# Performance work log

Hardware: AMD Instinct MI355X
Metric: run time of the kernel (lower is better)

Reference implementation:

```python
import jax, jax.numpy as jnp
import numpy as np

B, T, N, F_IN, F_OUT, H = 32, 32, 256, 32, 32, 256
NEG_SLOPE = 0.2  # GATConv default leaky-relu slope


def setup_inputs() -> dict:
    key = jax.random.key(0)
    ks = jax.random.split(key, 12)
    x = jax.random.normal(ks[0], (B, T, N, F_IN), dtype=jnp.float32)
    u = jax.random.uniform(ks[1], (B, T, N, N))
    w = jax.random.uniform(ks[2], (B, T, N, N))
    adj = jnp.where(u < 0.1, w, 0.0).astype(jnp.float32)
    # GAT params (heads=1, concat=False)
    W = jax.random.normal(ks[3], (F_IN, F_OUT), dtype=jnp.float32) / np.sqrt(F_IN)
    a_src = jax.random.normal(ks[4], (F_OUT,), dtype=jnp.float32) / np.sqrt(F_OUT)
    a_dst = jax.random.normal(ks[5], (F_OUT,), dtype=jnp.float32) / np.sqrt(F_OUT)
    gat_b = jnp.zeros((F_OUT,), dtype=jnp.float32)
    # LSTM params (PyTorch layout, gate order i,f,g,o)
    IN = N * F_OUT
    s = 1.0 / np.sqrt(H)
    W_ih = jax.random.uniform(ks[6], (4 * H, IN), minval=-s, maxval=s, dtype=jnp.float32)
    W_hh = jax.random.uniform(ks[7], (4 * H, H), minval=-s, maxval=s, dtype=jnp.float32)
    b_ih = jax.random.uniform(ks[8], (4 * H,), minval=-s, maxval=s, dtype=jnp.float32)
    b_hh = jax.random.uniform(ks[9], (4 * H,), minval=-s, maxval=s, dtype=jnp.float32)
    # output Linear
    Wo = jax.random.uniform(ks[10], (N, H), minval=-s, maxval=s, dtype=jnp.float32)
    bo = jax.random.uniform(ks[11], (N,), minval=-s, maxval=s, dtype=jnp.float32)
    return {"x": x, "adj": adj, "W": W, "a_src": a_src, "a_dst": a_dst,
            "gat_b": gat_b, "W_ih": W_ih, "W_hh": W_hh, "b_ih": b_ih,
            "b_hh": b_hh, "Wo": Wo, "bo": bo}


def _gat(x, adj, W, a_src, a_dst, gat_b):
    # batched over (B,T). h: [B,T,N,F_OUT]
    h = jnp.einsum('btnf,fo->btno', x, W)
    s_src = jnp.einsum('btno,o->btn', h, a_src)  # contribution of source node j
    s_dst = jnp.einsum('btno,o->btn', h, a_dst)  # contribution of target node i
    # e[i,j] = LeakyReLU(a_dst.h_i + a_src.h_j)
    e = jax.nn.leaky_relu(s_dst[..., :, None] + s_src[..., None, :], NEG_SLOPE)
    # edge (row=j -> col=i) exists iff adj[j,i] != 0; GATConv adds self-loops
    mask = (jnp.swapaxes(adj, -1, -2) != 0) | jnp.eye(N, dtype=bool)
    alpha = jax.nn.softmax(jnp.where(mask, e, -jnp.inf), axis=-1)  # softmax over sources j per target i
    return jnp.einsum('btij,btjo->btio', alpha, h) + gat_b


def _lstm_last(seq, W_ih, W_hh, b_ih, b_hh):
    # seq: [B,T,IN] -> last hidden state [B,H]
    def step(carry, x_t):
        h_prev, c_prev = carry
        gates = x_t @ W_ih.T + h_prev @ W_hh.T + (b_ih + b_hh)
        i, f, g, o = jnp.split(gates, 4, axis=-1)
        c = jax.nn.sigmoid(f) * c_prev + jax.nn.sigmoid(i) * jnp.tanh(g)
        h = jax.nn.sigmoid(o) * jnp.tanh(c)
        return (h, c), None
    init = (jnp.zeros((seq.shape[0], H), seq.dtype), jnp.zeros((seq.shape[0], H), seq.dtype))
    (h_last, _), _ = jax.lax.scan(step, init, jnp.swapaxes(seq, 0, 1))
    return h_last


def reference(x, adj, W, a_src, a_dst, gat_b, W_ih, W_hh, b_ih, b_hh, Wo, bo):
    gat_out = _gat(x, adj, W, a_src, a_dst, gat_b)            # [B,T,N,F_OUT]
    seq = gat_out.reshape(gat_out.shape[0], gat_out.shape[1], -1)  # [B,T,N*F_OUT]
    h_last = _lstm_last(seq, W_ih, W_hh, b_ih, b_hh)          # [B,H]
    return h_last @ Wo.T + bo                                  # [B,N]
```

## Files before the change

kernel.cpp:

```cpp
#include <hip/hip_runtime.h>
#include <cstdint>

constexpr int B_ = 32, T_ = 32, N_ = 256, FIN = 32, FOUT = 32, H_ = 256;
constexpr int IN_ = N_ * FOUT;
constexpr int G4  = 4 * H_;
constexpr int BT  = B_ * T_;
constexpr int KZ  = 8;
constexpr int NPACK = 4100;
#define NEG_SLOPE 0.2f

typedef _Float16 half8 __attribute__((ext_vector_type(8)));
typedef _Float16 h2    __attribute__((ext_vector_type(2)));
typedef float    f4    __attribute__((ext_vector_type(4)));

union U48 { uint4 u; half8 h; };

__device__ inline uint32_t pkh2(float a, float b) {
    union { uint32_t u; _Float16 h[2]; } z;
    z.h[0] = (_Float16)a; z.h[1] = (_Float16)b; return z.u;
}
__device__ inline float f16lo(uint32_t u){ union{uint32_t u; _Float16 h[2];} z; z.u=u; return (float)z.h[0]; }
__device__ inline float f16hi(uint32_t u){ union{uint32_t u; _Float16 h[2];} z; z.u=u; return (float)z.h[1]; }

__device__ inline float dot2f(uint32_t w, uint32_t h, float acc) {
    union { uint32_t u; h2 v; } a, b; a.u = w; b.u = h;
#if __has_builtin(__builtin_amdgcn_fdot2)
    return __builtin_amdgcn_fdot2(a.v, b.v, acc, false);
#else
    return acc + (float)a.v.x * (float)b.v.x + (float)a.v.y * (float)b.v.y;
#endif
}

__device__ inline void gload16(const void* g, void* l) {
    __builtin_amdgcn_global_load_lds(
        (const __attribute__((address_space(1))) void*)g,
        (__attribute__((address_space(3))) void*)l, 16, 0, 0);
}

__global__ __launch_bounds__(256) void gat_pack_kernel(
    const float* __restrict__ x, const float* __restrict__ adj,
    const float* __restrict__ W, const float* __restrict__ a_src,
    const float* __restrict__ a_dst, const float* __restrict__ gat_b,
    _Float16* __restrict__ seq,
    const float* __restrict__ Wih, const float* __restrict__ Whh,
    _Float16* __restrict__ wih_h, uint32_t* __restrict__ pwv,
    uint32_t* __restrict__ pwl, uint32_t* __restrict__ pws)
{
    if (blockIdx.x >= BT) {
        const int pid = blockIdx.x - BT;
        if (pid < 4096) {
            int idx = (pid * 256 + threadIdx.x) * 8;
            float4 v0 = *reinterpret_cast<const float4*>(Wih + idx);
            float4 v1 = *reinterpret_cast<const float4*>(Wih + idx + 4);
            half8 o;
            o[0]=(_Float16)v0.x; o[1]=(_Float16)v0.y; o[2]=(_Float16)v0.z; o[3]=(_Float16)v0.w;
            o[4]=(_Float16)v1.x; o[5]=(_Float16)v1.y; o[6]=(_Float16)v1.z; o[7]=(_Float16)v1.w;
            *reinterpret_cast<half8*>(wih_h + idx) = o;
        } else {
            int g = (pid - 4096) * 256 + threadIdx.x;
            const float* row = Whh + (size_t)g * H_;
            #pragma unroll
            for (int p = 0; p < 128; ++p) {
                float2 v = *reinterpret_cast<const float2*>(row + 2*p);
                uint32_t u = pkh2(v.x, v.y);
                if (p < 64) pwv[p * 1024 + g] = u;
                else if (p < 96) { int pp = p - 64; pwl[(pp >> 2) * 4096 + g * 4 + (pp & 3)] = u; }
                else             { int pp = p - 96; pws[(pp >> 2) * 4096 + g * 4 + (pp & 3)] = u; }
            }
        }
        return;
    }

    const int bt = blockIdx.x;
    const int i  = threadIdx.x;
    const int L  = i & 63, w = i >> 6;
    __shared__ __align__(16) uint32_t Pc[256 * 20];
    __shared__ __align__(16) _Float16 hT[32 * 264];
    __shared__ float ssrc[N_];
    __shared__ float linv[N_];
    __shared__ float asv[FOUT], adv[FOUT], gbv[FOUT];
    float* Ws = reinterpret_cast<float*>(Pc);

    for (int t = i; t < FIN * FOUT; t += 256) Ws[t] = W[t];
    if (i < FOUT) { asv[i] = a_src[i]; adv[i] = a_dst[i]; gbv[i] = gat_b[i]; }

    float xr[FIN];
    const float* xrow = x + ((size_t)bt * N_ + i) * FIN;
    #pragma unroll
    for (int f4i = 0; f4i < FIN / 4; ++f4i) {
        float4 v = reinterpret_cast<const float4*>(xrow)[f4i];
        xr[4*f4i] = v.x; xr[4*f4i+1] = v.y; xr[4*f4i+2] = v.z; xr[4*f4i+3] = v.w;
    }

    uint32_t msk[8];
    const float* adjcol = adj + (size_t)bt * N_ * N_ + i;
    #pragma unroll
    for (int gq = 0; gq < 8; ++gq) {
        uint32_t mm = ((i >> 5) == gq) ? (1u << (i & 31)) : 0u;
        #pragma unroll
        for (int u = 0; u < 32; ++u)
            mm |= (adjcol[(size_t)(gq * 32 + u) * N_] != 0.f ? 1u : 0u) << u;
        msk[gq] = mm;
    }
    __syncthreads();

    float hr[FOUT];
    #pragma unroll
    for (int k4 = 0; k4 < FOUT / 4; ++k4) {
        float ax = 0.f, ay = 0.f, az = 0.f, aw = 0.f;
        #pragma unroll
        for (int f = 0; f < FIN; ++f) {
            float4 w4 = *reinterpret_cast<const float4*>(&Ws[f*FOUT + 4*k4]);
            ax += xr[f]*w4.x; ay += xr[f]*w4.y; az += xr[f]*w4.z; aw += xr[f]*w4.w;
        }
        hr[4*k4] = ax; hr[4*k4+1] = ay; hr[4*k4+2] = az; hr[4*k4+3] = aw;
    }
    float ss = 0.f, sd = 0.f;
    #pragma unroll
    for (int k = 0; k < FOUT; ++k) { ss += hr[k]*asv[k]; sd += hr[k]*adv[k]; }
    #pragma unroll
    for (int k = 0; k < FOUT; ++k) hT[k*264 + i] = (_Float16)hr[k];
    ssrc[i] = ss;
    __syncthreads();

    float l = 0.f;
    f4 acc[4][2] = {};
    const int key = (i >> 3) & 3;
    const int m = L & 15, G = L >> 4;

    #pragma unroll
    for (int c = 0; c < 8; ++c) {
        const int j0 = c * 32;
        const uint32_t mm = msk[c];
        #pragma unroll
        for (int q = 0; q < 16; ++q) {
            int ja = j0 + 2*q, jb = ja + 1;
            float e0 = sd + ssrc[ja]; e0 = e0 > 0.f ? e0 : NEG_SLOPE * e0;
            float e1 = sd + ssrc[jb]; e1 = e1 > 0.f ? e1 : NEG_SLOPE * e1;
            float p0 = (mm & (1u << (2*q)))     ? __expf(e0) : 0.f;
            float p1 = (mm & (1u << (2*q + 1))) ? __expf(e1) : 0.f;
            l += p0 + p1;
            Pc[i*20 + (((q >> 2) ^ key) << 2) + (q & 3)] = pkh2(p0, p1);
        }
        U48 b0, b1;
        b0.h = *reinterpret_cast<const half8*>(&hT[m*264      + j0 + G*8]);
        b1.h = *reinterpret_cast<const half8*>(&hT[(m+16)*264 + j0 + G*8]);
        #pragma unroll
        for (int it = 0; it < 4; ++it) {
            int row = w*64 + it*16 + m;
            int rkey = (row >> 3) & 3;
            U48 a;
            a.u = reinterpret_cast<const uint4*>(&Pc[row*20])[G ^ rkey];
            acc[it][0] = __builtin_amdgcn_mfma_f32_16x16x32_f16(a.h, b0.h, acc[it][0], 0, 0, 0);
            acc[it][1] = __builtin_amdgcn_mfma_f32_16x16x32_f16(a.h, b1.h, acc[it][1], 0, 0, 0);
        }
    }
    linv[i] = 1.f / l;
    _Float16* obase = seq + (size_t)bt * IN_;
    #pragma unroll
    for (int it = 0; it < 4; ++it) {
        int ib = w*64 + it*16 + G*4;
        #pragma unroll
        for (int ot = 0; ot < 2; ++ot) {
            int o = ot*16 + m;
            float gb = gbv[o];
            #pragma unroll
            for (int r = 0; r < 4; ++r) {
                int row = ib + r;
                obase[row * FOUT + o] = (_Float16)(acc[it][ot][r] * linv[row] + gb);
            }
        }
    }
}

__global__ __launch_bounds__(256, 4) void gemm_kernel(
    const _Float16* __restrict__ A, const _Float16* __restrict__ Bh,
    float* __restrict__ Gp)
{
    __shared__ __align__(16) _Float16 As[128 * 32];
    __shared__ __align__(16) _Float16 Bs[128 * 32];
    const int t = threadIdx.x;
    const int L = t & 63, w = t >> 6;
    const int wm = w & 1, wn = w >> 1;
    const int m0 = blockIdx.y * 128, n0 = blockIdx.x * 128;
    const int kz = blockIdx.z * 1024;

    f4 acc[4][4] = {};
    const int q0 = t, q1 = t + 256;
    const int row0 = q0 >> 2, kc0 = q0 & 3;
    const int row1 = q1 >> 2, kc1 = q1 & 3;
    const int la = (L & 15) * 32 + (L >> 4) * 8;

    const _Float16* A0 = A + (size_t)(m0 + row0) * IN_ + kz + kc0 * 8;
    const _Float16* A1 = A + (size_t)(m0 + row1) * IN_ + kz + kc1 * 8;
    const _Float16* B0 = Bh + (size_t)(n0 + row0) * IN_ + kz + kc0 * 8;
    const _Float16* B1 = Bh + (size_t)(n0 + row1) * IN_ + kz + kc1 * 8;
    for (int kb = 0; kb < 1024; kb += 32) {
        __syncthreads();
        gload16(A0 + kb, &As[q0 * 8]);
        gload16(A1 + kb, &As[q1 * 8]);
        gload16(B0 + kb, &Bs[q0 * 8]);
        gload16(B1 + kb, &Bs[q1 * 8]);
        __syncthreads();
        half8 af[4], bf[4];
        #pragma unroll
        for (int mi = 0; mi < 4; ++mi)
            af[mi] = *reinterpret_cast<const half8*>(&As[(wm*64 + mi*16) * 32 + la]);
        #pragma unroll
        for (int ni = 0; ni < 4; ++ni)
            bf[ni] = *reinterpret_cast<const half8*>(&Bs[(wn*64 + ni*16) * 32 + la]);
        #pragma unroll
        for (int mi = 0; mi < 4; ++mi)
            #pragma unroll
            for (int ni = 0; ni < 4; ++ni)
                acc[mi][ni] = __builtin_amdgcn_mfma_f32_16x16x32_f16(
                    af[mi], bf[ni], acc[mi][ni], 0, 0, 0);
    }
    float* Gz = Gp + (size_t)blockIdx.z * BT * G4;
    const int cn = n0 + wn * 64 + (L & 15);
    const int rm = m0 + wm * 64 + (L >> 4) * 4;
    #pragma unroll
    for (int mi = 0; mi < 4; ++mi)
        #pragma unroll
        for (int ni = 0; ni < 4; ++ni)
            #pragma unroll
            for (int r = 0; r < 4; ++r)
                Gz[(size_t)(rm + mi*16 + r) * G4 + cn + ni*16] = acc[mi][ni][r];
}

__global__ __launch_bounds__(1024) void lstm_kernel(
    const float* __restrict__ Gp, const uint32_t* __restrict__ pwv,
    const uint32_t* __restrict__ pwl, const uint32_t* __restrict__ pws,
    const float* __restrict__ b_ih, const float* __restrict__ b_hh,
    const float* __restrict__ Wo, const float* __restrict__ bo,
    float* __restrict__ out)
{
    const int b = blockIdx.x;
    const int g = threadIdx.x;
    __shared__ __align__(16) uint32_t hsp[128];
    __shared__ float gsh[G4];
    __shared__ __align__(16) uint32_t wl[8 * 4096];

    uint32_t wv[64];
    #pragma unroll
    for (int p = 0; p < 64; ++p) wv[p] = pwv[p * 1024 + g];
    {
        const uint4* s = reinterpret_cast<const uint4*>(pwl);
        uint4* d = reinterpret_cast<uint4*>(wl);
        #pragma unroll
        for (int r = 0; r < 8; ++r) d[r * 1024 + g] = s[r * 1024 + g];
    }
    if (g < 128) hsp[g] = 0u;
    float c = 0.f;
    const float bias = b_ih[g] + b_hh[g];
    const size_t zs = (size_t)BT * G4;
    const float* Gb = Gp + (size_t)b * T_ * G4 + g;
    const uint4* pws4 = reinterpret_cast<const uint4*>(pws);
    const uint4* wl4  = reinterpret_cast<const uint4*>(wl);
    const uint4* hsp4 = reinterpret_cast<const uint4*>(hsp);

    float gcur = 0.f;
    #pragma unroll
    for (int z = 0; z < KZ; ++z) gcur += Gb[z * zs];
    __syncthreads();

    for (int t = 0; t < T_; ++t) {
        float acc = bias + gcur;
        float pf[KZ];
        const int tn = (t + 1 < T_) ? t + 1 : t;
        #pragma unroll
        for (int z = 0; z < KZ; ++z) pf[z] = Gb[(size_t)tn * G4 + z * zs];
        #pragma unroll
        for (int q = 0; q < 32; ++q) {
            uint4 h4 = hsp4[q];
            uint4 w4;
            if (q < 16) {
                w4.x = wv[4*q]; w4.y = wv[4*q+1]; w4.z = wv[4*q+2]; w4.w = wv[4*q+3];
            } else if (q < 24) {
                w4 = wl4[(q - 16) * 1024 + g];
            } else {
                w4 = pws4[(q - 24) * 1024 + g];
            }
            acc = dot2f(w4.x, h4.x, acc);
            acc = dot2f(w4.y, h4.y, acc);
            acc = dot2f(w4.z, h4.z, acc);
            acc = dot2f(w4.w, h4.w, acc);
        }
        gcur = ((pf[0]+pf[1]) + (pf[2]+pf[3])) + ((pf[4]+pf[5]) + (pf[6]+pf[7]));
        gsh[g] = acc;
        __syncthreads();
        if (g < H_) {
            float xi = gsh[g], xf = gsh[H_ + g], xg = gsh[2*H_ + g], xo = gsh[3*H_ + g];
            float si = 1.f / (1.f + __expf(-xi));
            float sf = 1.f / (1.f + __expf(-xf));
            float so = 1.f / (1.f + __expf(-xo));
            float eg = __expf(2.f * xg);
            float tg = 1.f - 2.f / (eg + 1.f);
            c = sf * c + si * tg;
            float ec = __expf(2.f * c);
            float th = 1.f - 2.f / (ec + 1.f);
            reinterpret_cast<_Float16*>(hsp)[g] = (_Float16)(so * th);
        }
        __syncthreads();
    }
    if (g < N_) {
        const float* worow = Wo + (size_t)g * H_;
        float o = bo[g];
        #pragma unroll
        for (int q = 0; q < 32; ++q) {
            uint4 hq = hsp4[q];
            float4 w0 = *reinterpret_cast<const float4*>(worow + q*8);
            float4 w1 = *reinterpret_cast<const float4*>(worow + q*8 + 4);
            o += w0.x * f16lo(hq.x) + w0.y * f16hi(hq.x)
               + w0.z * f16lo(hq.y) + w0.w * f16hi(hq.y)
               + w1.x * f16lo(hq.z) + w1.y * f16hi(hq.z)
               + w1.z * f16lo(hq.w) + w1.w * f16hi(hq.w);
        }
        out[(size_t)b * N_ + g] = o;
    }
}

extern "C" void kernel_launch(void* const* d_in, const int* in_sizes, int n_in,
                              void* d_out, int out_size, void* d_ws, size_t ws_size,
                              hipStream_t stream) {
    const float* x     = (const float*)d_in[0];
    const float* adj   = (const float*)d_in[1];
    const float* W     = (const float*)d_in[2];
    const float* a_src = (const float*)d_in[3];
    const float* a_dst = (const float*)d_in[4];
    const float* gat_b = (const float*)d_in[5];
    const float* W_ih  = (const float*)d_in[6];
    const float* W_hh  = (const float*)d_in[7];
    const float* b_ih  = (const float*)d_in[8];
    const float* b_hh  = (const float*)d_in[9];
    const float* Wo    = (const float*)d_in[10];
    const float* bo    = (const float*)d_in[11];
    float* out = (float*)d_out;

    _Float16* seq   = (_Float16*)d_ws;
    _Float16* wih_h = seq + (size_t)BT * IN_;
    float*    Gp    = (float*)(wih_h + (size_t)G4 * IN_);
    uint32_t* pwv   = (uint32_t*)(Gp + (size_t)KZ * BT * G4);
    uint32_t* pwl   = pwv + 64 * 1024;
    uint32_t* pws   = pwl + 32 * 1024;

    gat_pack_kernel<<<dim3(BT + NPACK), dim3(256), 0, stream>>>(
        x, adj, W, a_src, a_dst, gat_b, seq, W_ih, W_hh, wih_h, pwv, pwl, pws);
    gemm_kernel<<<dim3(8, 8, KZ), dim3(256), 0, stream>>>(seq, wih_h, Gp);
    lstm_kernel<<<dim3(B_), dim3(1024), 0, stream>>>(Gp, pwv, pwl, pws, b_ih, b_hh, Wo, bo, out);
}
```

Before: 653.5 us.

## Split adjacency mask building into a separate highly parallel kernel

Moves the adjacency-to-bitmask scan out of the per-(b,t) GAT block into the pack kernel, spreading each (b,t) adjacency over four blocks of 64 rows each. This raises parallelism for the dominant adjacency read (268MB), which was previously serialized per thread with 256 strided loads. The GAT kernel now reads a compact precomputed mask. It adds one extra kernel launch and a small mask buffer round-trip through memory.

After: 627.4 us. -4.0%, faster.

```diff
diff --git a/kernel.cpp b/kernel.cpp
--- a/kernel.cpp
+++ b/kernel.cpp
@@ -6,7 +6,6 @@
 constexpr int G4  = 4 * H_;
 constexpr int BT  = B_ * T_;
 constexpr int KZ  = 8;
-constexpr int NPACK = 4100;
 #define NEG_SLOPE 0.2f
 
 typedef _Float16 half8 __attribute__((ext_vector_type(8)));
@@ -37,40 +36,56 @@
         (__attribute__((address_space(3))) void*)l, 16, 0, 0);
 }
 
-__global__ __launch_bounds__(256) void gat_pack_kernel(
-    const float* __restrict__ x, const float* __restrict__ adj,
-    const float* __restrict__ W, const float* __restrict__ a_src,
-    const float* __restrict__ a_dst, const float* __restrict__ gat_b,
-    _Float16* __restrict__ seq,
+__global__ __launch_bounds__(256) void mask_pack_kernel(
+    const float* __restrict__ adj, uint32_t* __restrict__ msk,
     const float* __restrict__ Wih, const float* __restrict__ Whh,
     _Float16* __restrict__ wih_h, uint32_t* __restrict__ pwv,
     uint32_t* __restrict__ pwl, uint32_t* __restrict__ pws)
 {
-    if (blockIdx.x >= BT) {
-        const int pid = blockIdx.x - BT;
-        if (pid < 4096) {
-            int idx = (pid * 256 + threadIdx.x) * 8;
-            float4 v0 = *reinterpret_cast<const float4*>(Wih + idx);
-            float4 v1 = *reinterpret_cast<const float4*>(Wih + idx + 4);
-            half8 o;
-            o[0]=(_Float16)v0.x; o[1]=(_Float16)v0.y; o[2]=(_Float16)v0.z; o[3]=(_Float16)v0.w;
-            o[4]=(_Float16)v1.x; o[5]=(_Float16)v1.y; o[6]=(_Float16)v1.z; o[7]=(_Float16)v1.w;
-            *reinterpret_cast<half8*>(wih_h + idx) = o;
-        } else {
-            int g = (pid - 4096) * 256 + threadIdx.x;
-            const float* row = Whh + (size_t)g * H_;
-            #pragma unroll
-            for (int p = 0; p < 128; ++p) {
-                float2 v = *reinterpret_cast<const float2*>(row + 2*p);
-                uint32_t u = pkh2(v.x, v.y);
-                if (p < 64) pwv[p * 1024 + g] = u;
-                else if (p < 96) { int pp = p - 64; pwl[(pp >> 2) * 4096 + g * 4 + (pp & 3)] = u; }
-                else             { int pp = p - 96; pws[(pp >> 2) * 4096 + g * 4 + (pp & 3)] = u; }
-            }
-        }
-        return;
-    }
-
+    if (blockIdx.x < 4096) {
+        const int bt = blockIdx.x >> 2, js = blockIdx.x & 3;
+        const int i  = threadIdx.x;
+        const float* ac = adj + ((size_t)bt * N_ + js * 64) * N_ + i;
+        uint32_t m0 = 0u, m1 = 0u;
+        #pragma unroll
+        for (int u = 0; u < 32; ++u)
+            m0 |= (ac[(size_t)u * N_] != 0.f ? 1u : 0u) << u;
+        #pragma unroll
+        for (int u = 0; u < 32; ++u)
+            m1 |= (ac[(size_t)(32 + u) * N_] != 0.f ? 1u : 0u) << u;
+        const int gq0 = js * 2;
+        if ((i >> 5) == gq0)     m0 |= 1u << (i & 31);
+        if ((i >> 5) == gq0 + 1) m1 |= 1u << (i & 31);
+        msk[((size_t)bt * 8 + gq0)     * N_ + i] = m0;
+        msk[((size_t)bt * 8 + gq0 + 1) * N_ + i] = m1;
+    } else if (blockIdx.x < 8192) {
+        int idx = ((blockIdx.x - 4096) * 256 + threadIdx.x) * 8;
+        float4 v0 = *reinterpret_cast<const float4*>(Wih + idx);
+        float4 v1 = *reinterpret_cast<const float4*>(Wih + idx + 4);
+        half8 o;
+        o[0]=(_Float16)v0.x; o[1]=(_Float16)v0.y; o[2]=(_Float16)v0.z; o[3]=(_Float16)v0.w;
+        o[4]=(_Float16)v1.x; o[5]=(_Float16)v1.y; o[6]=(_Float16)v1.z; o[7]=(_Float16)v1.w;
+        *reinterpret_cast<half8*>(wih_h + idx) = o;
+    } else {
+        int g = (blockIdx.x - 8192) * 256 + threadIdx.x;
+        const float* row = Whh + (size_t)g * H_;
+        #pragma unroll
+        for (int p = 0; p < 128; ++p) {
+            float2 v = *reinterpret_cast<const float2*>(row + 2*p);
+            uint32_t u = pkh2(v.x, v.y);
+            if (p < 64) pwv[p * 1024 + g] = u;
+            else if (p < 96) { int pp = p - 64; pwl[(pp >> 2) * 4096 + g * 4 + (pp & 3)] = u; }
+            else             { int pp = p - 96; pws[(pp >> 2) * 4096 + g * 4 + (pp & 3)] = u; }
+        }
+    }
+}
+
+__global__ __launch_bounds__(256) void gat_kernel(
+    const float* __restrict__ x, const uint32_t* __restrict__ msk,
+    const float* __restrict__ W, const float* __restrict__ a_src,
+    const float* __restrict__ a_dst, const float* __restrict__ gat_b,
+    _Float16* __restrict__ seq)
+{
     const int bt = blockIdx.x;
     const int i  = threadIdx.x;
     const int L  = i & 63, w = i >> 6;
@@ -81,6 +96,11 @@
     __shared__ float asv[FOUT], adv[FOUT], gbv[FOUT];
     float* Ws = reinterpret_cast<float*>(Pc);
 
+    uint32_t msk_[8];
+    #pragma unroll
+    for (int gq = 0; gq < 8; ++gq)
+        msk_[gq] = msk[((size_t)bt * 8 + gq) * N_ + i];
+
     for (int t = i; t < FIN * FOUT; t += 256) Ws[t] = W[t];
     if (i < FOUT) { asv[i] = a_src[i]; adv[i] = a_dst[i]; gbv[i] = gat_b[i]; }
 
@@ -90,17 +110,6 @@
     for (int f4i = 0; f4i < FIN / 4; ++f4i) {
         float4 v = reinterpret_cast<const float4*>(xrow)[f4i];
         xr[4*f4i] = v.x; xr[4*f4i+1] = v.y; xr[4*f4i+2] = v.z; xr[4*f4i+3] = v.w;
-    }
-
-    uint32_t msk[8];
-    const float* adjcol = adj + (size_t)bt * N_ * N_ + i;
-    #pragma unroll
-    for (int gq = 0; gq < 8; ++gq) {
-        uint32_t mm = ((i >> 5) == gq) ? (1u << (i & 31)) : 0u;
-        #pragma unroll
-        for (int u = 0; u < 32; ++u)
-            mm |= (adjcol[(size_t)(gq * 32 + u) * N_] != 0.f ? 1u : 0u) << u;
-        msk[gq] = mm;
     }
     __syncthreads();
 
@@ -131,7 +140,7 @@
     #pragma unroll
     for (int c = 0; c < 8; ++c) {
         const int j0 = c * 32;
-        const uint32_t mm = msk[c];
+        const uint32_t mm = msk_[c];
         #pragma unroll
         for (int q = 0; q < 16; ++q) {
             int ja = j0 + 2*q, jb = ja + 1;
@@ -343,9 +352,12 @@
     uint32_t* pwv   = (uint32_t*)(Gp + (size_t)KZ * BT * G4);
     uint32_t* pwl   = pwv + 64 * 1024;
     uint32_t* pws   = pwl + 32 * 1024;
-
-    gat_pack_kernel<<<dim3(BT + NPACK), dim3(256), 0, stream>>>(
-        x, adj, W, a_src, a_dst, gat_b, seq, W_ih, W_hh, wih_h, pwv, pwl, pws);
+    uint32_t* msk   = pws + 32 * 1024;
+
+    mask_pack_kernel<<<dim3(8196), dim3(256), 0, stream>>>(
+        adj, msk, W_ih, W_hh, wih_h, pwv, pwl, pws);
+    gat_kernel<<<dim3(BT), dim3(256), 0, stream>>>(
+        x, msk, W, a_src, a_dst, gat_b, seq);
     gemm_kernel<<<dim3(8, 8, KZ), dim3(256), 0, stream>>>(seq, wih_h, Gp);
     lstm_kernel<<<dim3(B_), dim3(1024), 0, stream>>>(Gp, pwv, pwl, pws, b_ih, b_hh, Wo, bo, out);
 }
```
